# Kernel optimization log

Measured on AMD Instinct MI355X. Metric: run time of the kernel, lower is better.

The kernel has to match this reference:

```python
import jax, jax.numpy as jnp
import numpy as np

N_NODES = 20000
N_EDGES = 320000
NODE_DIM = 512
HIDDEN = 512
N_GRAPHS = 64


def setup_inputs() -> dict:
    key = jax.random.key(0)
    ks = jax.random.split(key, 12)
    s = 0.02
    return {
        "joint_x": jax.random.normal(ks[0], (N_NODES, NODE_DIM), jnp.float32),
        "joint_edge_index": jax.random.randint(ks[1], (2, N_EDGES), 0, N_NODES, dtype=jnp.int32),
        "joint_batch": jnp.sort(jax.random.randint(ks[2], (N_NODES,), 0, N_GRAPHS, dtype=jnp.int32)),
        "W_g1": jax.random.normal(ks[3], (NODE_DIM, HIDDEN), jnp.float32) * s,
        "b_g1": jnp.zeros((HIDDEN,), jnp.float32),
        "W_g2": jax.random.normal(ks[4], (HIDDEN, HIDDEN), jnp.float32) * s,
        "b_g2": jnp.zeros((HIDDEN,), jnp.float32),
        "W_c1": jax.random.normal(ks[5], (HIDDEN, HIDDEN // 2), jnp.float32) * s,
        "b_c1": jnp.zeros((HIDDEN // 2,), jnp.float32),
        "W_c2": jax.random.normal(ks[6], (HIDDEN // 2, 1), jnp.float32) * s,
        "b_c2": jnp.zeros((1,), jnp.float32),
    }


def _gin_layer(h, src, dst, W, b):
    # GINConv(nn=Linear, eps=0): nn((1+eps)*x_i + sum_{j->i} x_j)
    agg = jax.ops.segment_sum(h[src], dst, num_segments=N_NODES)  # [N, D]
    return (h + agg) @ W + b


def reference(joint_x, joint_edge_index, joint_batch, W_g1, b_g1, W_g2, b_g2, W_c1, b_c1, W_c2, b_c2):
    src, dst = joint_edge_index[0], joint_edge_index[1]
    h = _gin_layer(joint_x, src, dst, W_g1, b_g1)  # [N, HIDDEN]
    h = _gin_layer(h, src, dst, W_g2, b_g2)        # [N, HIDDEN]
    pooled = jax.ops.segment_sum(h, joint_batch, num_segments=N_GRAPHS)  # [G, HIDDEN]
    z = jax.nn.relu(pooled @ W_c1 + b_c1)
    score = z @ W_c2 + b_c2                        # [G, 1]
    return jax.nn.sigmoid(score).squeeze(-1)       # [G]
```

## Files before the change

### kernel.cpp

```cpp
#include <hip/hip_runtime.h>
#include <math.h>

constexpr int N_NODES = 20000;
constexpr int DIM = 512;
constexpr int NG = 64;
constexpr int CAP = 64;
constexpr int KCH = 128;
constexpr int NCHUNK = (N_NODES + KCH - 1) / KCH;
constexpr int RSPLIT = 4;
constexpr int CPS = (NCHUNK + RSPLIT - 1) / RSPLIT;
constexpr int CGS = 32;
constexpr int CSTR = 16;
constexpr int NODE_BLOCKS = (N_NODES + 3) / 4;
constexpr int INIT_BLOCKS = (N_NODES + 255) / 256;
constexpr int GEMM_TILES = 17 * 4;
constexpr int EPT = 2;
constexpr int EDGE_BLOCKS = (320000 + 256 * EPT - 1) / (256 * EPT);

__device__ __forceinline__ int lower_bound_i(const int* __restrict__ a, int n, int v) {
  int lo = 0, hi = n;
  while (lo < hi) {
    int mid = (lo + hi) >> 1;
    if (a[mid] < v) lo = mid + 1; else hi = mid;
  }
  return lo;
}

__global__ __launch_bounds__(256) void node_init(const int* __restrict__ batch,
                                                 int* __restrict__ cursor,
                                                 float* __restrict__ ng,
                                                 float* __restrict__ cgpad, int n_nodes) {
  int node = blockIdx.x * 256 + threadIdx.x;
  if (node < n_nodes) cursor[(size_t)node * CSTR] = 0;
  if (blockIdx.x == 0 && threadIdx.x < 64) {
    int gg = threadIdx.x;
    int s0 = lower_bound_i(batch, n_nodes, gg);
    int e0 = lower_bound_i(batch, n_nodes, gg + 1);
    ng[gg] = (float)(e0 - s0);
    cgpad[gg * CGS] = 0.f;
  }
}

__device__ void gemm_stack_tile(const float* __restrict__ A0, const float* __restrict__ extra,
                                const float* __restrict__ B, float* __restrict__ C,
                                int M, int N, int K, int R0, int tile,
                                float* As, float* Bs, int tid) {
  int bm = (tile >> 2) * 32;
  int bn = (tile & 3) * 64;
  int tx = tid & 15;
  int ty = tid >> 4;
  int ar = tid >> 3;
  int ac = (tid & 7) * 2;
  int br = tid >> 4;
  int bc = (tid & 15) * 4;
  float acc[2][4] = {};
  for (int k0 = 0; k0 < K; k0 += 16) {
    int row = bm + ar;
    float2 av = make_float2(0.f, 0.f);
    if (row < R0)       av = *(const float2*)(A0 + (size_t)row * K + k0 + ac);
    else if (row == R0) av = *(const float2*)(extra + k0 + ac);
    As[(ac + 0) * 34 + ar] = av.x;
    As[(ac + 1) * 34 + ar] = av.y;
    *(float4*)&Bs[br * 68 + bc] = *(const float4*)(B + (size_t)(k0 + br) * N + bn + bc);
    __syncthreads();
#pragma unroll
    for (int kk = 0; kk < 16; ++kk) {
      float2 a01 = *(const float2*)&As[kk * 34 + ty * 2];
      float4 bv  = *(const float4*)&Bs[kk * 68 + tx * 4];
      acc[0][0] = fmaf(a01.x, bv.x, acc[0][0]); acc[0][1] = fmaf(a01.x, bv.y, acc[0][1]);
      acc[0][2] = fmaf(a01.x, bv.z, acc[0][2]); acc[0][3] = fmaf(a01.x, bv.w, acc[0][3]);
      acc[1][0] = fmaf(a01.y, bv.x, acc[1][0]); acc[1][1] = fmaf(a01.y, bv.y, acc[1][1]);
      acc[1][2] = fmaf(a01.y, bv.z, acc[1][2]); acc[1][3] = fmaf(a01.y, bv.w, acc[1][3]);
    }
    __syncthreads();
  }
#pragma unroll
  for (int i = 0; i < 2; ++i) {
    int m = bm + ty * 2 + i;
    if (m >= M) continue;
    *(float4*)&C[(size_t)m * N + bn + tx * 4] =
        make_float4(acc[i][0], acc[i][1], acc[i][2], acc[i][3]);
  }
}

__global__ __launch_bounds__(256) void fill_and_Q(const int* __restrict__ srcI,
                                                  const int* __restrict__ dstI,
                                                  const int* __restrict__ batch,
                                                  int* __restrict__ cursor,
                                                  int* __restrict__ edst,
                                                  float* __restrict__ cgpad,
                                                  const float* __restrict__ Wg2,
                                                  const float* __restrict__ bg2,
                                                  const float* __restrict__ Wc1,
                                                  float* __restrict__ Q, int n_edges) {
  __shared__ float As[16 * 34];
  __shared__ float Bs[16 * 68];
  __shared__ int hist[64];
  int b = blockIdx.x;
  int t = threadIdx.x;
  if (b < EDGE_BLOCKS) {
    if (t < 64) hist[t] = 0;
    __syncthreads();
    int base = b * (256 * EPT) + t;
    int s[EPT], d[EPT], c[EPT];
    bool v[EPT];
#pragma unroll
    for (int u = 0; u < EPT; ++u) {
      int i = base + u * 256;
      v[u] = i < n_edges;
      s[u] = v[u] ? srcI[i] : 0;
    }
#pragma unroll
    for (int u = 0; u < EPT; ++u) {
      int i = base + u * 256;
      d[u] = v[u] ? dstI[i] : 0;
    }
#pragma unroll
    for (int u = 0; u < EPT; ++u)
      if (v[u]) c[u] = atomicAdd(&cursor[(size_t)s[u] * CSTR], 1);
#pragma unroll
    for (int u = 0; u < EPT; ++u)
      if (v[u]) edst[(size_t)s[u] * CAP + c[u]] = d[u];
#pragma unroll
    for (int u = 0; u < EPT; ++u)
      if (v[u]) atomicAdd(&hist[batch[d[u]]], 1);
    __syncthreads();
    if (t < 64 && hist[t] != 0) atomicAdd(&cgpad[t * CGS], (float)hist[t]);
  } else {
    gemm_stack_tile(Wg2, bg2, Wc1, Q, 513, 256, 512, 512, b - EDGE_BLOCKS, As, Bs, t);
  }
}

__global__ __launch_bounds__(256) void build_wT(const int* __restrict__ batch,
                                                const int* __restrict__ deg,
                                                const int* __restrict__ edst,
                                                float* __restrict__ wT, int n_nodes) {
  int node = blockIdx.x * 4 + (threadIdx.x >> 6);
  int g = threadIdx.x & 63;
  if (node >= n_nodes) return;
  int end = deg[(size_t)node * CSTR];
  const int* nb = edst + (size_t)node * CAP;
  float acc = (batch[node] == g) ? 1.f : 0.f;
  int i = 0;
  for (; i + 7 < end; i += 8) {
    int d0 = nb[i], d1 = nb[i + 1], d2 = nb[i + 2], d3 = nb[i + 3];
    int d4 = nb[i + 4], d5 = nb[i + 5], d6 = nb[i + 6], d7 = nb[i + 7];
    int b0 = batch[d0], b1 = batch[d1], b2 = batch[d2], b3 = batch[d3];
    int b4 = batch[d4], b5 = batch[d5], b6 = batch[d6], b7 = batch[d7];
    acc += ((float)(b0 == g) + (float)(b1 == g)) + ((float)(b2 == g) + (float)(b3 == g)) +
           ((float)(b4 == g) + (float)(b5 == g)) + ((float)(b6 == g) + (float)(b7 == g));
  }
  for (; i < end; ++i) acc += (float)(batch[nb[i]] == g);
  wT[(size_t)node * 64 + g] = acc;
}

__global__ __launch_bounds__(256) void cT_and_P(const float* __restrict__ wT,
                                                const int* __restrict__ deg,
                                                const int* __restrict__ edst,
                                                float* __restrict__ cT,
                                                const float* __restrict__ Wg1,
                                                const float* __restrict__ bg1,
                                                const float* __restrict__ Q,
                                                float* __restrict__ P, int n_nodes) {
  __shared__ float As[16 * 34];
  __shared__ float Bs[16 * 68];
  int b = blockIdx.x;
  int t = threadIdx.x;
  if (b < NODE_BLOCKS) {
    int node = b * 4 + (t >> 6);
    int g = t & 63;
    if (node >= n_nodes) return;
    float acc = wT[(size_t)node * 64 + g];
    int end = deg[(size_t)node * CSTR];
    const int* nb = edst + (size_t)node * CAP;
    int i = 0;
    for (; i + 7 < end; i += 8) {
      int d0 = nb[i], d1 = nb[i + 1], d2 = nb[i + 2], d3 = nb[i + 3];
      int d4 = nb[i + 4], d5 = nb[i + 5], d6 = nb[i + 6], d7 = nb[i + 7];
      float v0 = wT[(size_t)d0 * 64 + g], v1 = wT[(size_t)d1 * 64 + g];
      float v2 = wT[(size_t)d2 * 64 + g], v3 = wT[(size_t)d3 * 64 + g];
      float v4 = wT[(size_t)d4 * 64 + g], v5 = wT[(size_t)d5 * 64 + g];
      float v6 = wT[(size_t)d6 * 64 + g], v7 = wT[(size_t)d7 * 64 + g];
      acc += ((v0 + v1) + (v2 + v3)) + ((v4 + v5) + (v6 + v7));
    }
    for (; i + 3 < end; i += 4) {
      int d0 = nb[i], d1 = nb[i + 1], d2 = nb[i + 2], d3 = nb[i + 3];
      acc += wT[(size_t)d0 * 64 + g] + wT[(size_t)d1 * 64 + g] +
             wT[(size_t)d2 * 64 + g] + wT[(size_t)d3 * 64 + g];
    }
    for (; i < end; ++i) acc += wT[(size_t)nb[i] * 64 + g];
    cT[(size_t)node * 64 + g] = acc;
  } else {
    gemm_stack_tile(Wg1, bg1, Q, P, 513, 256, 512, 512, b - NODE_BLOCKS, As, Bs, t);
  }
}

__global__ __launch_bounds__(256) void ugemm(const float* __restrict__ x,
                                             const float* __restrict__ cT,
                                             float* __restrict__ Upart) {
  __shared__ float sc[KCH][64];
  int t = threadIdx.x;
  int k0 = blockIdx.y * KCH;
  int kmax = (N_NODES - k0) < KCH ? (N_NODES - k0) : KCH;
  {
    const float4* src = (const float4*)(cT + (size_t)k0 * 64);
    float4* dst = (float4*)(&sc[0][0]);
    int limit4 = kmax * 16;
    for (int i = t; i < limit4; i += 256) dst[i] = src[i];
  }
  __syncthreads();
  int lane = t & 63;
  int slice = t >> 6;
  int n2 = blockIdx.x * 64 + lane;
  const float2* x2 = (const float2*)x;
  float2 acc[16];
#pragma unroll
  for (int j = 0; j < 16; ++j) acc[j] = make_float2(0.f, 0.f);
  for (int kk = 0; kk < kmax; kk += 4) {
    float2 xv[4];
#pragma unroll
    for (int u = 0; u < 4; ++u)
      xv[u] = x2[(size_t)(k0 + kk + u) * 256 + n2];
#pragma unroll
    for (int u = 0; u < 4; ++u) {
      const float4* cp = (const float4*)&sc[kk + u][slice * 16];
      float4 c0 = cp[0], c1 = cp[1], c2 = cp[2], c3 = cp[3];
      float2 xu = xv[u];
      acc[0].x  = fmaf(c0.x, xu.x, acc[0].x);  acc[0].y  = fmaf(c0.x, xu.y, acc[0].y);
      acc[1].x  = fmaf(c0.y, xu.x, acc[1].x);  acc[1].y  = fmaf(c0.y, xu.y, acc[1].y);
      acc[2].x  = fmaf(c0.z, xu.x, acc[2].x);  acc[2].y  = fmaf(c0.z, xu.y, acc[2].y);
      acc[3].x  = fmaf(c0.w, xu.x, acc[3].x);  acc[3].y  = fmaf(c0.w, xu.y, acc[3].y);
      acc[4].x  = fmaf(c1.x, xu.x, acc[4].x);  acc[4].y  = fmaf(c1.x, xu.y, acc[4].y);
      acc[5].x  = fmaf(c1.y, xu.x, acc[5].x);  acc[5].y  = fmaf(c1.y, xu.y, acc[5].y);
      acc[6].x  = fmaf(c1.z, xu.x, acc[6].x);  acc[6].y  = fmaf(c1.z, xu.y, acc[6].y);
      acc[7].x  = fmaf(c1.w, xu.x, acc[7].x);  acc[7].y  = fmaf(c1.w, xu.y, acc[7].y);
      acc[8].x  = fmaf(c2.x, xu.x, acc[8].x);  acc[8].y  = fmaf(c2.x, xu.y, acc[8].y);
      acc[9].x  = fmaf(c2.y, xu.x, acc[9].x);  acc[9].y  = fmaf(c2.y, xu.y, acc[9].y);
      acc[10].x = fmaf(c2.z, xu.x, acc[10].x); acc[10].y = fmaf(c2.z, xu.y, acc[10].y);
      acc[11].x = fmaf(c2.w, xu.x, acc[11].x); acc[11].y = fmaf(c2.w, xu.y, acc[11].y);
      acc[12].x = fmaf(c3.x, xu.x, acc[12].x); acc[12].y = fmaf(c3.x, xu.y, acc[12].y);
      acc[13].x = fmaf(c3.y, xu.x, acc[13].x); acc[13].y = fmaf(c3.y, xu.y, acc[13].y);
      acc[14].x = fmaf(c3.z, xu.x, acc[14].x); acc[14].y = fmaf(c3.z, xu.y, acc[14].y);
      acc[15].x = fmaf(c3.w, xu.x, acc[15].x); acc[15].y = fmaf(c3.w, xu.y, acc[15].y);
    }
  }
  float2* up = (float2*)Upart;
#pragma unroll
  for (int j = 0; j < 16; ++j) {
    int g = slice * 16 + j;
    up[((size_t)blockIdx.y * 64 + g) * 256 + n2] = acc[j];
  }
}

__global__ __launch_bounds__(128) void reduce_U(const float* __restrict__ Upart,
                                                float* __restrict__ Ured) {
  int g = blockIdx.x;
  int s = blockIdx.y;
  int t = threadIdx.x;
  int c0 = s * CPS;
  int c1 = (c0 + CPS < NCHUNK) ? c0 + CPS : NCHUNK;
  const float4* up = (const float4*)Upart;
  float4 acc = make_float4(0.f, 0.f, 0.f, 0.f);
  for (int c = c0; c < c1; ++c) {
    float4 v = up[((size_t)c * 64 + g) * 128 + t];
    acc.x += v.x; acc.y += v.y; acc.z += v.z; acc.w += v.w;
  }
  ((float4*)Ured)[((size_t)s * 64 + g) * 128 + t] = acc;
}

__global__ __launch_bounds__(256) void head(const float* __restrict__ Ured,
                                            const float* __restrict__ P,
                                            const float* __restrict__ Q,
                                            const float* __restrict__ ng,
                                            const float* __restrict__ cgpad,
                                            const float* __restrict__ bc1,
                                            const float* __restrict__ Wc2,
                                            const float* __restrict__ bc2,
                                            float* __restrict__ out) {
  int g = blockIdx.x;
  int j = threadIdx.x;
  const float* Wc = P;
  const float* v1 = P + (size_t)512 * 256;
  const float* v2 = Q + (size_t)512 * 256;
  __shared__ float p[512];
  float s0 = 0.f, s1 = 0.f;
#pragma unroll
  for (int s = 0; s < RSPLIT; ++s) {
    s0 += Ured[((size_t)s * 64 + g) * DIM + j];
    s1 += Ured[((size_t)s * 64 + g) * DIM + 256 + j];
  }
  p[j] = s0;
  p[j + 256] = s1;
  __syncthreads();
  float cg = ng[g] + cgpad[g * CGS];
  float acc = bc1[j] + cg * v1[j] + ng[g] * v2[j];
  for (int k = 0; k < 512; ++k) acc = fmaf(p[k], Wc[k * 256 + j], acc);
  float z = fmaxf(acc, 0.f);
  float part = z * Wc2[j];
  for (int off = 32; off > 0; off >>= 1) part += __shfl_down(part, off, 64);
  __shared__ float red[4];
  if ((j & 63) == 0) red[j >> 6] = part;
  __syncthreads();
  if (j == 0) {
    float tot = red[0] + red[1] + red[2] + red[3] + bc2[0];
    out[g] = 1.f / (1.f + expf(-tot));
  }
}

extern "C" void kernel_launch(void* const* d_in, const int* in_sizes, int n_in,
                              void* d_out, int out_size, void* d_ws, size_t ws_size,
                              hipStream_t stream) {
  const float* x    = (const float*)d_in[0];
  const int*   ei   = (const int*)d_in[1];
  const int*   batch= (const int*)d_in[2];
  const float* Wg1  = (const float*)d_in[3];
  const float* bg1  = (const float*)d_in[4];
  const float* Wg2  = (const float*)d_in[5];
  const float* bg2  = (const float*)d_in[6];
  const float* Wc1  = (const float*)d_in[7];
  const float* bc1  = (const float*)d_in[8];
  const float* Wc2  = (const float*)d_in[9];
  const float* bc2  = (const float*)d_in[10];
  float* out = (float*)d_out;

  int n_edges = in_sizes[1] / 2;
  int n_nodes = in_sizes[2];
  const int* srcI = ei;
  const int* dstI = ei + n_edges;

  char* ws = (char*)d_ws;
  size_t off = 0;
  auto alloc = [&](size_t bytes) { char* p = ws + off; off += (bytes + 255) & ~(size_t)255; return p; };
  float* wT    = (float*)alloc((size_t)N_NODES * 64 * sizeof(float));
  float* cT    = (float*)alloc((size_t)N_NODES * 64 * sizeof(float));
  float* Upart = (float*)alloc((size_t)NCHUNK * 64 * DIM * sizeof(float));
  float* Ured  = (float*)alloc((size_t)RSPLIT * 64 * DIM * sizeof(float));
  float* Q     = (float*)alloc((size_t)513 * 256 * sizeof(float));
  float* P     = (float*)alloc((size_t)513 * 256 * sizeof(float));
  float* ng    = (float*)alloc(NG * sizeof(float));
  float* cgpad = (float*)alloc(NG * CGS * sizeof(float));
  int* cursor  = (int*)alloc((size_t)N_NODES * CSTR * sizeof(int));
  int* edst    = (int*)alloc((size_t)N_NODES * CAP * sizeof(int));

  node_init<<<INIT_BLOCKS, 256, 0, stream>>>(batch, cursor, ng, cgpad, n_nodes);
  fill_and_Q<<<EDGE_BLOCKS + GEMM_TILES, 256, 0, stream>>>(srcI, dstI, batch, cursor, edst,
                                                           cgpad, Wg2, bg2, Wc1, Q, n_edges);
  build_wT<<<NODE_BLOCKS, 256, 0, stream>>>(batch, cursor, edst, wT, n_nodes);
  cT_and_P<<<NODE_BLOCKS + GEMM_TILES, 256, 0, stream>>>(wT, cursor, edst, cT,
                                                         Wg1, bg1, Q, P, n_nodes);
  ugemm<<<dim3(4, NCHUNK), 256, 0, stream>>>(x, cT, Upart);
  reduce_U<<<dim3(64, RSPLIT), 128, 0, stream>>>(Upart, Ured);
  head<<<NG, 256, 0, stream>>>(Ured, P, Q, ng, cgpad, bc1, Wc2, bc2, out);
}
```

Baseline: 244.5 us.

## Split small weight GEMMs along K and schedule their blocks first in fused kernels

The two weight-product GEMMs (Q = [Wg2;bg2]·Wc1 and P = [Wg1;bg1]·Q) are split into two K halves, each written to its own partial buffer. The next GEMM sums the Q partials when loading B, and the head kernel sums the P and Q partials on read. GEMM blocks are moved to the front of the fused launches so these long-latency tiles start first instead of trailing behind the edge and node blocks. This shortens the critical path of each GEMM tile at the cost of twice the buffer memory and extra loads in the head kernel.

```diff
diff --git a/kernel.cpp b/kernel.cpp
--- a/kernel.cpp
+++ b/kernel.cpp
@@ -14,6 +14,8 @@
 constexpr int NODE_BLOCKS = (N_NODES + 3) / 4;
 constexpr int INIT_BLOCKS = (N_NODES + 255) / 256;
 constexpr int GEMM_TILES = 17 * 4;
+constexpr int KSPLIT_TILES = GEMM_TILES * 2;
+constexpr int PQ_ELEMS = 513 * 256;
 constexpr int EPT = 2;
 constexpr int EDGE_BLOCKS = (320000 + 256 * EPT - 1) / (256 * EPT);
 
@@ -42,8 +44,9 @@
 }
 
 __device__ void gemm_stack_tile(const float* __restrict__ A0, const float* __restrict__ extra,
-                                const float* __restrict__ B, float* __restrict__ C,
-                                int M, int N, int K, int R0, int tile,
+                                const float* __restrict__ B, const float* __restrict__ B2,
+                                float* __restrict__ C,
+                                int N, int K, int R0, int tile, int kbeg, int kend,
                                 float* As, float* Bs, int tid) {
   int bm = (tile >> 2) * 32;
   int bn = (tile & 3) * 64;
@@ -54,30 +57,36 @@
   int br = tid >> 4;
   int bc = (tid & 15) * 4;
   float acc[2][4] = {};
-  for (int k0 = 0; k0 < K; k0 += 16) {
+  for (int k0 = kbeg; k0 < kend; k0 += 16) {
     int row = bm + ar;
     float2 av = make_float2(0.f, 0.f);
     if (row < R0)       av = *(const float2*)(A0 + (size_t)row * K + k0 + ac);
     else if (row == R0) av = *(const float2*)(extra + k0 + ac);
     As[(ac + 0) * 34 + ar] = av.x;
     As[(ac + 1) * 34 + ar] = av.y;
-    *(float4*)&Bs[br * 68 + bc] = *(const float4*)(B + (size_t)(k0 + br) * N + bn + bc);
+    size_t boff = (size_t)(k0 + br) * N + bn + bc;
+    float4 bv = *(const float4*)(B + boff);
+    if (B2) {
+      float4 b2 = *(const float4*)(B2 + boff);
+      bv.x += b2.x; bv.y += b2.y; bv.z += b2.z; bv.w += b2.w;
+    }
+    *(float4*)&Bs[br * 68 + bc] = bv;
     __syncthreads();
 #pragma unroll
     for (int kk = 0; kk < 16; ++kk) {
       float2 a01 = *(const float2*)&As[kk * 34 + ty * 2];
-      float4 bv  = *(const float4*)&Bs[kk * 68 + tx * 4];
-      acc[0][0] = fmaf(a01.x, bv.x, acc[0][0]); acc[0][1] = fmaf(a01.x, bv.y, acc[0][1]);
-      acc[0][2] = fmaf(a01.x, bv.z, acc[0][2]); acc[0][3] = fmaf(a01.x, bv.w, acc[0][3]);
-      acc[1][0] = fmaf(a01.y, bv.x, acc[1][0]); acc[1][1] = fmaf(a01.y, bv.y, acc[1][1]);
-      acc[1][2] = fmaf(a01.y, bv.z, acc[1][2]); acc[1][3] = fmaf(a01.y, bv.w, acc[1][3]);
+      float4 b4  = *(const float4*)&Bs[kk * 68 + tx * 4];
+      acc[0][0] = fmaf(a01.x, b4.x, acc[0][0]); acc[0][1] = fmaf(a01.x, b4.y, acc[0][1]);
+      acc[0][2] = fmaf(a01.x, b4.z, acc[0][2]); acc[0][3] = fmaf(a01.x, b4.w, acc[0][3]);
+      acc[1][0] = fmaf(a01.y, b4.x, acc[1][0]); acc[1][1] = fmaf(a01.y, b4.y, acc[1][1]);
+      acc[1][2] = fmaf(a01.y, b4.z, acc[1][2]); acc[1][3] = fmaf(a01.y, b4.w, acc[1][3]);
     }
     __syncthreads();
   }
 #pragma unroll
   for (int i = 0; i < 2; ++i) {
     int m = bm + ty * 2 + i;
-    if (m >= M) continue;
+    if (m > R0) continue;
     *(float4*)&C[(size_t)m * N + bn + tx * 4] =
         make_float4(acc[i][0], acc[i][1], acc[i][2], acc[i][3]);
   }
@@ -98,10 +107,16 @@
   __shared__ int hist[64];
   int b = blockIdx.x;
   int t = threadIdx.x;
-  if (b < EDGE_BLOCKS) {
+  if (b < KSPLIT_TILES) {
+    int ks = b & 1;
+    int tile = b >> 1;
+    gemm_stack_tile(Wg2, bg2, Wc1, nullptr, Q + (size_t)ks * PQ_ELEMS,
+                    256, 512, 512, tile, ks * 256, ks * 256 + 256, As, Bs, t);
+  } else {
+    int eb = b - KSPLIT_TILES;
     if (t < 64) hist[t] = 0;
     __syncthreads();
-    int base = b * (256 * EPT) + t;
+    int base = eb * (256 * EPT) + t;
     int s[EPT], d[EPT], c[EPT];
     bool v[EPT];
 #pragma unroll
@@ -126,8 +141,6 @@
       if (v[u]) atomicAdd(&hist[batch[d[u]]], 1);
     __syncthreads();
     if (t < 64 && hist[t] != 0) atomicAdd(&cgpad[t * CGS], (float)hist[t]);
-  } else {
-    gemm_stack_tile(Wg2, bg2, Wc1, Q, 513, 256, 512, 512, b - EDGE_BLOCKS, As, Bs, t);
   }
 }
 
@@ -166,8 +179,13 @@
   __shared__ float Bs[16 * 68];
   int b = blockIdx.x;
   int t = threadIdx.x;
-  if (b < NODE_BLOCKS) {
-    int node = b * 4 + (t >> 6);
+  if (b < KSPLIT_TILES) {
+    int ks = b & 1;
+    int tile = b >> 1;
+    gemm_stack_tile(Wg1, bg1, Q, Q + PQ_ELEMS, P + (size_t)ks * PQ_ELEMS,
+                    256, 512, 512, tile, ks * 256, ks * 256 + 256, As, Bs, t);
+  } else {
+    int node = (b - KSPLIT_TILES) * 4 + (t >> 6);
     int g = t & 63;
     if (node >= n_nodes) return;
     float acc = wT[(size_t)node * 64 + g];
@@ -190,8 +208,6 @@
     }
     for (; i < end; ++i) acc += wT[(size_t)nb[i] * 64 + g];
     cT[(size_t)node * 64 + g] = acc;
-  } else {
-    gemm_stack_tile(Wg1, bg1, Q, P, 513, 256, 512, 512, b - NODE_BLOCKS, As, Bs, t);
   }
 }
 
@@ -279,9 +295,12 @@
                                             float* __restrict__ out) {
   int g = blockIdx.x;
   int j = threadIdx.x;
-  const float* Wc = P;
-  const float* v1 = P + (size_t)512 * 256;
-  const float* v2 = Q + (size_t)512 * 256;
+  const float* Wc0 = P;
+  const float* Wc1p = P + (size_t)PQ_ELEMS;
+  const float* v1a = P + (size_t)512 * 256;
+  const float* v1b = P + (size_t)PQ_ELEMS + (size_t)512 * 256;
+  const float* v2a = Q + (size_t)512 * 256;
+  const float* v2b = Q + (size_t)PQ_ELEMS + (size_t)512 * 256;
   __shared__ float p[512];
   float s0 = 0.f, s1 = 0.f;
 #pragma unroll
@@ -293,8 +312,11 @@
   p[j + 256] = s1;
   __syncthreads();
   float cg = ng[g] + cgpad[g * CGS];
-  float acc = bc1[j] + cg * v1[j] + ng[g] * v2[j];
-  for (int k = 0; k < 512; ++k) acc = fmaf(p[k], Wc[k * 256 + j], acc);
+  float acc = bc1[j] + cg * (v1a[j] + v1b[j]) + ng[g] * (v2a[j] + v2b[j]);
+  for (int k = 0; k < 512; ++k) {
+    float w = Wc0[k * 256 + j] + Wc1p[k * 256 + j];
+    acc = fmaf(p[k], w, acc);
+  }
   float z = fmaxf(acc, 0.f);
   float part = z * Wc2[j];
   for (int off = 32; off > 0; off >>= 1) part += __shfl_down(part, off, 64);
@@ -335,19 +357,19 @@
   float* cT    = (float*)alloc((size_t)N_NODES * 64 * sizeof(float));
   float* Upart = (float*)alloc((size_t)NCHUNK * 64 * DIM * sizeof(float));
   float* Ured  = (float*)alloc((size_t)RSPLIT * 64 * DIM * sizeof(float));
-  float* Q     = (float*)alloc((size_t)513 * 256 * sizeof(float));
-  float* P     = (float*)alloc((size_t)513 * 256 * sizeof(float));
+  float* Q     = (float*)alloc((size_t)2 * PQ_ELEMS * sizeof(float));
+  float* P     = (float*)alloc((size_t)2 * PQ_ELEMS * sizeof(float));
   float* ng    = (float*)alloc(NG * sizeof(float));
   float* cgpad = (float*)alloc(NG * CGS * sizeof(float));
   int* cursor  = (int*)alloc((size_t)N_NODES * CSTR * sizeof(int));
   int* edst    = (int*)alloc((size_t)N_NODES * CAP * sizeof(int));
 
   node_init<<<INIT_BLOCKS, 256, 0, stream>>>(batch, cursor, ng, cgpad, n_nodes);
-  fill_and_Q<<<EDGE_BLOCKS + GEMM_TILES, 256, 0, stream>>>(srcI, dstI, batch, cursor, edst,
-                                                           cgpad, Wg2, bg2, Wc1, Q, n_edges);
+  fill_and_Q<<<KSPLIT_TILES + EDGE_BLOCKS, 256, 0, stream>>>(srcI, dstI, batch, cursor, edst,
+                                                             cgpad, Wg2, bg2, Wc1, Q, n_edges);
   build_wT<<<NODE_BLOCKS, 256, 0, stream>>>(batch, cursor, edst, wT, n_nodes);
-  cT_and_P<<<NODE_BLOCKS + GEMM_TILES, 256, 0, stream>>>(wT, cursor, edst, cT,
-                                                         Wg1, bg1, Q, P, n_nodes);
+  cT_and_P<<<KSPLIT_TILES + NODE_BLOCKS, 256, 0, stream>>>(wT, cursor, edst, cT,
+                                                           Wg1, bg1, Q, P, n_nodes);
   ugemm<<<dim3(4, NCHUNK), 256, 0, stream>>>(x, cT, Upart);
   reduce_U<<<dim3(64, RSPLIT), 128, 0, stream>>>(Upart, Ured);
   head<<<NG, 256, 0, stream>>>(Ured, P, Q, ng, cgpad, bc1, Wc2, bc2, out);
```

Result: faster. 224.5 us (-8.2%).
